# Optimization experiments

Measured on AMD Instinct MI355X. Metric: run time of the kernel, lower is better.

## Reference

```python
import jax, jax.numpy as jnp
import numpy as np

E = 512
H = 8
D = E // H
WIN = 128  # mask_window_size


def setup_inputs() -> dict:
    key = jax.random.key(0)
    k1, k2, k3, k4, k5 = jax.random.split(key, 5)
    B, L = 2, 4096
    s = 1.0 / np.sqrt(E)
    return {
        "x": jax.random.normal(k1, (B, L, E), dtype=jnp.float32),
        "in_proj_w": jax.random.normal(k2, (3 * E, E), dtype=jnp.float32) * s,
        "in_proj_b": jax.random.normal(k3, (3 * E,), dtype=jnp.float32) * 0.02,
        "out_w": jax.random.normal(k4, (E, E), dtype=jnp.float32) * s,
        "out_b": jax.random.normal(k5, (E,), dtype=jnp.float32) * 0.02,
    }


def reference(x, in_proj_w, in_proj_b, out_w, out_b):
    B, L, _ = x.shape
    # fused qkv projection (torch MultiheadAttention in_proj): x @ W.T + b
    qkv = jnp.einsum("ble,fe->blf", x, in_proj_w) + in_proj_b  # [B,L,3E]
    q, k, v = jnp.split(qkv, 3, axis=-1)
    # [B,H,L,D]
    q = q.reshape(B, L, H, D).transpose(0, 2, 1, 3)
    k = k.reshape(B, L, H, D).transpose(0, 2, 1, 3)
    v = v.reshape(B, L, H, D).transpose(0, 2, 1, 3)
    scores = jnp.einsum("bhqd,bhkd->bhqk", q, k) / jnp.sqrt(jnp.float32(D))
    # (diagonal stays blocked — faithful to the original gen_mask quirk)
    idx = jnp.arange(L)
    dist = jnp.abs(idx[:, None] - idx[None, :])
    blocked = (dist > WIN) | (dist == 0)  # [L,L]
    scores = jnp.where(blocked[None, None], -jnp.inf, scores)
    attn = jax.nn.softmax(scores, axis=-1)  # [B,H,L,L]
    out = jnp.einsum("bhqk,bhkd->bhqd", attn, v)  # [B,H,L,D]
    out = out.transpose(0, 2, 1, 3).reshape(B, L, E)
    return jnp.einsum("ble,fe->blf", out, out_w) + out_b
```

## Files before the change

### kernel.cpp

```cpp
#include <hip/hip_runtime.h>
#include <math.h>

#define E_DIM 512
#define H_DIM 8
#define WIN 128
#define L_SEQ 4096
#define B_SZ 2

typedef unsigned short ushort_t;
typedef unsigned int uint_t;
typedef __attribute__((ext_vector_type(8))) __bf16 bf16x8;
typedef __attribute__((ext_vector_type(4))) float f32x4;

__device__ __forceinline__ ushort_t f2bf(float f) {
    uint_t u = __float_as_uint(f);
    u = u + 0x7fffu + ((u >> 16) & 1u);
    return (ushort_t)(u >> 16);
}
__device__ __forceinline__ uint_t pk2bf(float lo, float hi) {
    uint_t r;
    asm("v_cvt_pk_bf16_f32 %0, %1, %2" : "=v"(r) : "v"(lo), "v"(hi));
    return r;
}

__device__ __forceinline__ void gload16(const ushort_t* g, ushort_t* l) {
    __builtin_amdgcn_global_load_lds(
        (const __attribute__((address_space(1))) void*)g,
        (__attribute__((address_space(3))) void*)l,
        16, 0, 0);
}


__global__ __launch_bounds__(256) void convertX(
    const float* __restrict__ x,  ushort_t* __restrict__ xh,
    const float* __restrict__ w1, ushort_t* __restrict__ w1h,
    const float* __restrict__ w2, ushort_t* __restrict__ w2h) {
    int sg = blockIdx.x * 256 + threadIdx.x;
    const float* src; ushort_t* dh;
    if (sg < 524288)      { src = x;  dh = xh; }
    else if (sg < 622592) { src = w1; dh = w1h; sg -= 524288; }
    else                  { src = w2; dh = w2h; sg -= 622592; }
    const int tile = sg >> 6, slot = sg & 63;
    const int row = (tile >> 4) * 16 + (slot & 15);
    const int k   = (tile & 15) * 32 + (slot >> 4) * 8;
    const float4 v0 = *(const float4*)&src[(size_t)row * 512 + k];
    const float4 v1 = *(const float4*)&src[(size_t)row * 512 + k + 4];
    uint4 ov;
    ov.x = pk2bf(v0.x, v0.y);
    ov.y = pk2bf(v0.z, v0.w);
    ov.z = pk2bf(v1.x, v1.y);
    ov.w = pk2bf(v1.z, v1.w);
    *(uint4*)(dh + (size_t)sg * 8) = ov;
}

__global__ __launch_bounds__(256) void gemm_qkv(
    const ushort_t* __restrict__ Ah,
    const ushort_t* __restrict__ Wh,
    const float* __restrict__ bias,
    ushort_t* __restrict__ qTh,
    ushort_t* __restrict__ kTh,
    ushort_t* __restrict__ vTh) {
    __shared__ __align__(16) ushort_t sAh[2][8 * 512];
    __shared__ __align__(16) ushort_t sWh[2][8 * 512];

    const int tid = threadIdx.x, lane = tid & 63, w = tid >> 6;
    const int wm = w & 1, wn = w >> 1, ln = lane & 15, quad = lane >> 4;
    const int bx = blockIdx.x, by = blockIdx.y;
    const int lo8 = lane * 8;
    const int wu = __builtin_amdgcn_readfirstlane(w);

    f32x4 acc[4][4];
    const f32x4 zero = {0.f, 0.f, 0.f, 0.f};
    #pragma unroll
    for (int i = 0; i < 4; i++)
        #pragma unroll
        for (int j = 0; j < 4; j++) acc[i][j] = zero;

    const ushort_t* pb[4];
    ushort_t* db0[4];
    ushort_t* db1[4];
    #pragma unroll
    for (int t = 0; t < 4; t++) {
        const int g = wu * 4 + t;
        if (g < 8) {
            pb[t] = Ah + ((size_t)(bx * 8 + g) * 16) * 512;
            db0[t] = &sAh[0][g * 512]; db1[t] = &sAh[1][g * 512];
        } else {
            const int u = g - 8;
            pb[t] = Wh + ((size_t)(by * 8 + u) * 16) * 512;
            db0[t] = &sWh[0][u * 512]; db1[t] = &sWh[1][u * 512];
        }
    }

    #pragma unroll
    for (int t = 0; t < 4; t++)
        gload16(pb[t] + lo8, db0[t]);

    for (int kt = 0; kt < 16; kt++) {
        __syncthreads();
        if (kt < 15) {
            const int koff = (kt + 1) * 512;
            if ((kt + 1) & 1) {
                #pragma unroll
                for (int t = 0; t < 4; t++) gload16(pb[t] + koff + lo8, db1[t]);
            } else {
                #pragma unroll
                for (int t = 0; t < 4; t++) gload16(pb[t] + koff + lo8, db0[t]);
            }
        }
        const int cb = kt & 1;
        bf16x8 fah[4];
        #pragma unroll
        for (int i = 0; i < 4; i++)
            fah[i] = *(const bf16x8*)&sAh[cb][(wm * 4 + i) * 512 + lo8];
        #pragma unroll
        for (int j = 0; j < 4; j++) {
            const bf16x8 fbh = *(const bf16x8*)&sWh[cb][(wn * 4 + j) * 512 + lo8];
            #pragma unroll
            for (int i = 0; i < 4; i++)
                acc[i][j] = __builtin_amdgcn_mfma_f32_16x16x32_bf16(fah[i], fbh, acc[i][j], 0, 0, 0);
        }
    }

    const int b = bx >> 5;
    const int h = 2 * (by & 3) + wn;
    if (by < 8) {
        ushort_t* dh = (by < 4) ? qTh : kTh;
        #pragma unroll
        for (int i = 0; i < 4; i++) {
            const int rt = (bx & 31) * 8 + wm * 4 + i;
            const size_t tb = ((size_t)(b * 8 + h) * 256 + rt) * 2;
            #pragma unroll
            for (int j = 0; j < 4; j++) {
                const float bv = bias[by * 128 + wn * 64 + j * 16 + ln];
                const size_t tile = tb + (j >> 1);
                const uint_t pa = pk2bf(acc[i][j][0] + bv, acc[i][j][1] + bv);
                const uint_t pc = pk2bf(acc[i][j][2] + bv, acc[i][j][3] + bv);
                const int slot0 = ((j * 2 + (ln >> 3)) & 3) * 16 + quad * 4;
                const size_t idx0 = tile * 512 + slot0 * 8 + (ln & 7);
                dh[idx0]      = (ushort_t)pa;
                dh[idx0 + 8]  = (ushort_t)(pa >> 16);
                dh[idx0 + 16] = (ushort_t)pc;
                dh[idx0 + 24] = (ushort_t)(pc >> 16);
            }
        }
    } else {
        const int kwin = (bx & 31) * 2 + wm;
        #pragma unroll
        for (int i = 0; i < 4; i++) {
            const int kk = i >> 1;
            #pragma unroll
            for (int j = 0; j < 4; j++) {
                const float bv = bias[by * 128 + wn * 64 + j * 16 + ln];
                const size_t tile = (((size_t)(b * 8 + h) * 64 + kwin) * 4 + j) * 2 + kk;
                const uint_t pa = pk2bf(acc[i][j][0] + bv, acc[i][j][1] + bv);
                const uint_t pc = pk2bf(acc[i][j][2] + bv, acc[i][j][3] + bv);
                const int slot = ((i & 1) * 2 + (quad >> 1)) * 16 + ln;
                uint2 ov; ov.x = pa; ov.y = pc;
                *(uint2*)&vTh[tile * 512 + slot * 8 + (quad & 1) * 4] = ov;
            }
        }
    }
}

__global__ __launch_bounds__(512) void attn_mfma(
    const ushort_t* __restrict__ qTh,
    const ushort_t* __restrict__ kTh,
    const ushort_t* __restrict__ vTh,
    ushort_t* __restrict__ outh) {
    __shared__ __align__(16) ushort_t sKh[2][8 * 512];
    __shared__ __align__(16) ushort_t sV [2][8 * 512];
    __shared__ __align__(16) ushort_t sP [16 * 512];

    const int qs = blockIdx.x * 128;
    const int h = blockIdx.y, b = blockIdx.z;
    const int bh = b * 8 + h;
    const int tid = threadIdx.x, lane = tid & 63;
    const int w = tid >> 6, ln = lane & 15, quad = lane >> 4;
    const int lo8 = lane * 8;

    bf16x8 qf[2];
    {
        const size_t qt = ((size_t)bh * 256 + (qs >> 4) + w) * 2;
        qf[0] = *(const bf16x8*)(qTh + (qt + 0) * 512 + lo8);
        qf[1] = *(const bf16x8*)(qTh + (qt + 1) * 512 + lo8);
    }

    f32x4 oacc[4];
    const f32x4 zero = {0.f, 0.f, 0.f, 0.f};
    #pragma unroll
    for (int dt = 0; dt < 4; dt++) oacc[dt] = zero;
    float m_run = -1e30f, l_run = 0.f;

    const float cscale = 0.125f * 1.44269504f;
    const int qlo = qs + 16 * w;
    const int q = qlo + ln;
    const int lo_b = (q - WIN) < 0 ? 0 : (q - WIN);
    const int hi_b = (q + WIN) > (L_SEQ - 1) ? (L_SEQ - 1) : (q + WIN);

    {
        if (w < 4) {
            int st = (qs >> 4) - 8 + w;
            st = st < 0 ? 0 : (st > 255 ? 255 : st);
            const size_t kb = ((size_t)bh * 256 + st) * 2 * 512 + lo8;
            gload16(kTh + kb,       &sKh[0][(w * 2 + 0) * 512]);
            gload16(kTh + kb + 512, &sKh[0][(w * 2 + 1) * 512]);
        } else {
            const int u = w - 4;
            int vw = (qs >> 6) - 2;
            vw = vw < 0 ? 0 : (vw > 63 ? 63 : vw);
            const size_t vb = (((size_t)bh * 64 + vw) * 4 + u) * 2 * 512 + lo8;
            gload16(vTh + vb,       &sV[0][(u * 2 + 0) * 512]);
            gload16(vTh + vb + 512, &sV[0][(u * 2 + 1) * 512]);
        }
    }

    for (int kt = 0; kt < 6; kt++) {
        const int ks = qs - 128 + kt * 64;

        __syncthreads();

        if (kt < 5) {
            const int nb = (kt + 1) & 1;
            if (w < 4) {
                int st = (qs >> 4) - 8 + (kt + 1) * 4 + w;
                st = st < 0 ? 0 : (st > 255 ? 255 : st);
                const size_t kb = ((size_t)bh * 256 + st) * 2 * 512 + lo8;
                gload16(kTh + kb,       &sKh[nb][(w * 2 + 0) * 512]);
                gload16(kTh + kb + 512, &sKh[nb][(w * 2 + 1) * 512]);
            } else {
                const int u = w - 4;
                int vw = (qs >> 6) - 2 + kt + 1;
                vw = vw < 0 ? 0 : (vw > 63 ? 63 : vw);
                const size_t vb = (((size_t)bh * 64 + vw) * 4 + u) * 2 * 512 + lo8;
                gload16(vTh + vb,       &sV[nb][(u * 2 + 0) * 512]);
                gload16(vTh + vb + 512, &sV[nb][(u * 2 + 1) * 512]);
            }
        }
        const int cb = kt & 1;

        bool dead[4];
        #pragma unroll
        for (int jt = 0; jt < 4; jt++) {
            const int klo = ks + 16 * jt;
            dead[jt] = (klo > qlo + 15 + WIN) || (klo + 15 < qlo - WIN) ||
                       (klo >= L_SEQ) || (klo + 15 < 0);
        }
        const bool hdead0 = dead[0] && dead[1];
        const bool hdead1 = dead[2] && dead[3];
        const bool ktAlive = !(hdead0 && hdead1);

        if (ktAlive) {
            f32x4 st4[4];
            __builtin_amdgcn_s_setprio(1);
            #pragma unroll
            for (int jt = 0; jt < 4; jt++) {
                f32x4 a = zero;
                if (!dead[jt]) {
                    #pragma unroll
                    for (int kk = 0; kk < 2; kk++) {
                        const bf16x8 kh = *(const bf16x8*)&sKh[cb][(jt * 2 + kk) * 512 + lo8];
                        a = __builtin_amdgcn_mfma_f32_16x16x32_bf16(kh, qf[kk], a, 0, 0, 0);
                    }
                }
                st4[jt] = a;
            }
            __builtin_amdgcn_s_setprio(0);

            float mkr = -INFINITY;
            #pragma unroll
            for (int jt = 0; jt < 4; jt++)
                if (!dead[jt])
                    #pragma unroll
                    for (int r = 0; r < 4; r++)
                        mkr = fmaxf(mkr, st4[jt][r]);
            mkr = fmaxf(mkr, __shfl_xor(mkr, 16));
            mkr = fmaxf(mkr, __shfl_xor(mkr, 32));

            const float mnew = fmaxf(m_run, mkr * cscale);
            const bool raised = mnew > m_run;
            const float alpha = exp2f(m_run - mnew);
            m_run = mnew;

            float ps = 0.f;
            #pragma unroll
            for (int jt = 0; jt < 4; jt++) {
                if (!dead[jt]) {
                    #pragma unroll
                    for (int r = 0; r < 4; r++) {
                        const int kcol = ks + jt * 16 + quad * 4 + r;
                        const bool ok = (kcol >= lo_b) && (kcol <= hi_b) && (kcol != q);
                        float p = exp2f(st4[jt][r] * cscale - mnew);
                        p = ok ? p : 0.f;
                        st4[jt][r] = p;
                        ps += p;
                    }
                }
            }
            ps += __shfl_xor(ps, 16);
            ps += __shfl_xor(ps, 32);
            l_run = l_run * alpha + ps;

            if (__any(raised)) {
                float ar[4];
                #pragma unroll
                for (int r = 0; r < 4; r++)
                    ar[r] = __shfl(alpha, quad * 4 + r);
                #pragma unroll
                for (int dt = 0; dt < 4; dt++)
                    #pragma unroll
                    for (int r = 0; r < 4; r++)
                        oacc[dt][r] *= ar[r];
            }

            #pragma unroll
            for (int jt = 0; jt < 4; jt++) {
                const bool hd = (jt < 2) ? hdead0 : hdead1;
                if (!hd) {
                    uint2 pw;
                    if (!dead[jt]) {
                        pw.x = pk2bf(st4[jt][0], st4[jt][1]);
                        pw.y = pk2bf(st4[jt][2], st4[jt][3]);
                    } else { pw.x = 0u; pw.y = 0u; }
                    const int slot = ((jt & 1) * 2 + (quad >> 1)) * 16 + ln;
                    *(uint2*)&sP[w * 1024 + (jt >> 1) * 512 + slot * 8 + (quad & 1) * 4] = pw;
                }
            }

            #pragma unroll
            for (int kk = 0; kk < 2; kk++) {
                const bool hd = (kk == 0) ? hdead0 : hdead1;
                if (!hd) {
                    const bf16x8 pf = *(const bf16x8*)&sP[w * 1024 + kk * 512 + lo8];
                    __builtin_amdgcn_s_setprio(1);
                    #pragma unroll
                    for (int dt = 0; dt < 4; dt++) {
                        const bf16x8 vf = *(const bf16x8*)&sV[cb][(dt * 2 + kk) * 512 + lo8];
                        oacc[dt] = __builtin_amdgcn_mfma_f32_16x16x32_bf16(pf, vf, oacc[dt], 0, 0, 0);
                    }
                    __builtin_amdgcn_s_setprio(0);
                }
            }
        }
    }

    const int Rt = ((b * L_SEQ + qs) >> 4) + w;
    float invl[4];
    #pragma unroll
    for (int r = 0; r < 4; r++) {
        const float lr = __shfl(l_run, quad * 4 + r);
        invl[r] = __builtin_amdgcn_rcpf(lr);
    }
    #pragma unroll
    for (int dt = 0; dt < 4; dt++) {
        const uint_t pa = pk2bf(oacc[dt][0] * invl[0], oacc[dt][1] * invl[1]);
        const uint_t pc = pk2bf(oacc[dt][2] * invl[2], oacc[dt][3] * invl[3]);
        const int tile = Rt * 16 + h * 2 + (dt >> 1);
        const int slot0 = ((dt & 1) * 2 + (ln >> 3)) * 16 + quad * 4;
        const size_t idx0 = (size_t)tile * 512 + slot0 * 8 + (ln & 7);
        outh[idx0]      = (ushort_t)pa;
        outh[idx0 + 8]  = (ushort_t)(pa >> 16);
        outh[idx0 + 16] = (ushort_t)pc;
        outh[idx0 + 24] = (ushort_t)(pc >> 16);
    }
}

__global__ __launch_bounds__(512) void gemm_out(
    const ushort_t* __restrict__ Ah,
    const ushort_t* __restrict__ Wh,
    const float* __restrict__ bias, float* __restrict__ C) {
    __shared__ __align__(16) ushort_t sAh[2][16 * 512];
    __shared__ __align__(16) ushort_t sWh[2][8 * 512];

    const int tid = threadIdx.x, lane = tid & 63, w = tid >> 6;
    const int wm = w & 3, wn = w >> 2, ln = lane & 15, quad = lane >> 4;
    const int bx = blockIdx.x, by = blockIdx.y;
    const int lo8 = lane * 8;
    const int wu = __builtin_amdgcn_readfirstlane(w);

    f32x4 acc[2][2];
    const f32x4 zero = {0.f, 0.f, 0.f, 0.f};
    #pragma unroll
    for (int i = 0; i < 2; i++)
        #pragma unroll
        for (int j = 0; j < 2; j++) acc[i][j] = zero;

    const ushort_t* pb[3];
    ushort_t* db0[3];
    ushort_t* db1[3];
    #pragma unroll
    for (int t = 0; t < 3; t++) {
        const int g = wu * 3 + t;
        if (g < 16) {
            pb[t] = Ah + ((size_t)(bx * 8 + (g >> 1)) * 16 + (g & 1)) * 512;
            db0[t] = &sAh[0][g * 512]; db1[t] = &sAh[1][g * 512];
        } else {
            const int u = g - 16;
            pb[t] = Wh + ((size_t)(by * 4 + (u >> 1)) * 16 + (u & 1)) * 512;
            db0[t] = &sWh[0][u * 512]; db1[t] = &sWh[1][u * 512];
        }
    }

    #pragma unroll
    for (int t = 0; t < 3; t++)
        gload16(pb[t] + lo8, db0[t]);

    for (int KT = 0; KT < 8; KT++) {
        __syncthreads();
        if (KT < 7) {
            const int koff = (KT + 1) * 1024;
            if ((KT + 1) & 1) {
                #pragma unroll
                for (int t = 0; t < 3; t++) gload16(pb[t] + koff + lo8, db1[t]);
            } else {
                #pragma unroll
                for (int t = 0; t < 3; t++) gload16(pb[t] + koff + lo8, db0[t]);
            }
        }
        const int cb = KT & 1;
        #pragma unroll
        for (int ks = 0; ks < 2; ks++) {
            bf16x8 fah[2];
            #pragma unroll
            for (int i = 0; i < 2; i++)
                fah[i] = *(const bf16x8*)&sAh[cb][((wm * 2 + i) * 2 + ks) * 512 + lo8];
            #pragma unroll
            for (int j = 0; j < 2; j++) {
                const bf16x8 fbh = *(const bf16x8*)&sWh[cb][((wn * 2 + j) * 2 + ks) * 512 + lo8];
                #pragma unroll
                for (int i = 0; i < 2; i++)
                    acc[i][j] = __builtin_amdgcn_mfma_f32_16x16x32_bf16(fah[i], fbh, acc[i][j], 0, 0, 0);
            }
        }
    }

    #pragma unroll
    for (int i = 0; i < 2; i++) {
        const int row0 = bx * 128 + wm * 32 + i * 16 + quad * 4;
        #pragma unroll
        for (int j = 0; j < 2; j++) {
            const int col = by * 64 + wn * 32 + j * 16 + ln;
            const float bv = bias[col];
            #pragma unroll
            for (int r = 0; r < 4; r++)
                C[(size_t)(row0 + r) * E_DIM + col] = acc[i][j][r] + bv;
        }
    }
}

extern "C" void kernel_launch(void* const* d_in, const int* in_sizes, int n_in,
                              void* d_out, int out_size, void* d_ws, size_t ws_size,
                              hipStream_t stream) {
    const float* x         = (const float*)d_in[0];
    const float* in_proj_w = (const float*)d_in[1];
    const float* in_proj_b = (const float*)d_in[2];
    const float* out_w     = (const float*)d_in[3];
    const float* out_b     = (const float*)d_in[4];
    float* out = (float*)d_out;

    const int N = B_SZ * L_SEQ;
    const size_t NE = (size_t)N * E_DIM;

    char* p = (char*)d_ws;
    ushort_t* xh  = (ushort_t*)p; p += NE * 2;
    ushort_t* w1h = (ushort_t*)p; p += (size_t)3 * E_DIM * E_DIM * 2;
    ushort_t* w2h = (ushort_t*)p; p += (size_t)E_DIM * E_DIM * 2;
    ushort_t* qTh = (ushort_t*)p; p += NE * 2;
    ushort_t* kTh = (ushort_t*)p; p += NE * 2;
    ushort_t* vTh = (ushort_t*)p; p += NE * 2;
    ushort_t* ath = (ushort_t*)p; p += NE * 2;

    convertX<<<2560, 256, 0, stream>>>(x, xh, in_proj_w, w1h, out_w, w2h);

    gemm_qkv<<<dim3(64, 12), 256, 0, stream>>>(
        xh, w1h, in_proj_b, qTh, kTh, vTh);

    attn_mfma<<<dim3(L_SEQ / 128, H_DIM, B_SZ), 512, 0, stream>>>(
        qTh, kTh, vTh, ath);

    gemm_out<<<dim3(64, 8), 512, 0, stream>>>(
        ath, w2h, out_b, out);
}
```

Baseline: 130.6 us.

## Triple-buffer LDS loads in QKV and output GEMMs with explicit vmcnt waits

Both projection GEMMs move from double to triple buffering in shared memory, prefetching two K-tiles ahead. The blanket __syncthreads is replaced with a partial s_waitcnt vmcnt wait followed by s_barrier, so the load of the tile after next stays in flight while the current tile is computed. This is meant to hide more global-to-LDS latency. It costs 50% more LDS per block, which may lower occupancy, and the hand-tuned vmcnt counts must exactly match how many loads each thread issues.

Measured after the change: 127.1 us. 2.7% less time.

```diff
diff --git a/kernel.cpp b/kernel.cpp
--- a/kernel.cpp
+++ b/kernel.cpp
@@ -60,8 +60,8 @@
     ushort_t* __restrict__ qTh,
     ushort_t* __restrict__ kTh,
     ushort_t* __restrict__ vTh) {
-    __shared__ __align__(16) ushort_t sAh[2][8 * 512];
-    __shared__ __align__(16) ushort_t sWh[2][8 * 512];
+    __shared__ __align__(16) ushort_t sAh[3][8 * 512];
+    __shared__ __align__(16) ushort_t sWh[3][8 * 512];
 
     const int tid = threadIdx.x, lane = tid & 63, w = tid >> 6;
     const int wm = w & 1, wn = w >> 1, ln = lane & 15, quad = lane >> 4;
@@ -69,6 +69,10 @@
     const int lo8 = lane * 8;
     const int wu = __builtin_amdgcn_readfirstlane(w);
 
+    const ushort_t* sA0 = &sAh[0][0];
+    const ushort_t* sW0 = &sWh[0][0];
+    const int BUF = 8 * 512;
+
     f32x4 acc[4][4];
     const f32x4 zero = {0.f, 0.f, 0.f, 0.f};
     #pragma unroll
@@ -77,45 +81,51 @@
         for (int j = 0; j < 4; j++) acc[i][j] = zero;
 
     const ushort_t* pb[4];
-    ushort_t* db0[4];
-    ushort_t* db1[4];
+    ushort_t* db[4];
     #pragma unroll
     for (int t = 0; t < 4; t++) {
         const int g = wu * 4 + t;
         if (g < 8) {
             pb[t] = Ah + ((size_t)(bx * 8 + g) * 16) * 512;
-            db0[t] = &sAh[0][g * 512]; db1[t] = &sAh[1][g * 512];
+            db[t] = &sAh[0][g * 512];
         } else {
             const int u = g - 8;
             pb[t] = Wh + ((size_t)(by * 8 + u) * 16) * 512;
-            db0[t] = &sWh[0][u * 512]; db1[t] = &sWh[1][u * 512];
-        }
-    }
-
-    #pragma unroll
-    for (int t = 0; t < 4; t++)
-        gload16(pb[t] + lo8, db0[t]);
-
+            db[t] = &sWh[0][u * 512];
+        }
+    }
+
+    #pragma unroll
+    for (int t = 0; t < 4; t++) gload16(pb[t] + lo8, db[t]);
+    #pragma unroll
+    for (int t = 0; t < 4; t++) gload16(pb[t] + 512 + lo8, db[t] + BUF);
+
+    int bw = 2, br = 0;
     for (int kt = 0; kt < 16; kt++) {
-        __syncthreads();
-        if (kt < 15) {
-            const int koff = (kt + 1) * 512;
-            if ((kt + 1) & 1) {
-                #pragma unroll
-                for (int t = 0; t < 4; t++) gload16(pb[t] + koff + lo8, db1[t]);
-            } else {
-                #pragma unroll
-                for (int t = 0; t < 4; t++) gload16(pb[t] + koff + lo8, db0[t]);
-            }
-        }
-        const int cb = kt & 1;
+        if (kt < 15) asm volatile("s_waitcnt vmcnt(4) lgkmcnt(0)" ::: "memory");
+        else         asm volatile("s_waitcnt vmcnt(0) lgkmcnt(0)" ::: "memory");
+        __builtin_amdgcn_s_barrier();
+        __builtin_amdgcn_sched_barrier(0);
+
+        if (kt < 14) {
+            const int koff = (kt + 2) * 512;
+            const int bwo = bw * BUF;
+            #pragma unroll
+            for (int t = 0; t < 4; t++)
+                gload16(pb[t] + koff + lo8, db[t] + bwo);
+            bw = (bw == 2) ? 0 : bw + 1;
+        }
+
+        const int bro = br * BUF;
+        br = (br == 2) ? 0 : br + 1;
+
         bf16x8 fah[4];
         #pragma unroll
         for (int i = 0; i < 4; i++)
-            fah[i] = *(const bf16x8*)&sAh[cb][(wm * 4 + i) * 512 + lo8];
+            fah[i] = *(const bf16x8*)&sA0[bro + (wm * 4 + i) * 512 + lo8];
         #pragma unroll
         for (int j = 0; j < 4; j++) {
-            const bf16x8 fbh = *(const bf16x8*)&sWh[cb][(wn * 4 + j) * 512 + lo8];
+            const bf16x8 fbh = *(const bf16x8*)&sW0[bro + (wn * 4 + j) * 512 + lo8];
             #pragma unroll
             for (int i = 0; i < 4; i++)
                 acc[i][j] = __builtin_amdgcn_mfma_f32_16x16x32_bf16(fah[i], fbh, acc[i][j], 0, 0, 0);
@@ -369,8 +379,8 @@
     const ushort_t* __restrict__ Ah,
     const ushort_t* __restrict__ Wh,
     const float* __restrict__ bias, float* __restrict__ C) {
-    __shared__ __align__(16) ushort_t sAh[2][16 * 512];
-    __shared__ __align__(16) ushort_t sWh[2][8 * 512];
+    __shared__ __align__(16) ushort_t sAh[3][16 * 512];
+    __shared__ __align__(16) ushort_t sWh[3][8 * 512];
 
     const int tid = threadIdx.x, lane = tid & 63, w = tid >> 6;
     const int wm = w & 3, wn = w >> 2, ln = lane & 15, quad = lane >> 4;
@@ -378,6 +388,10 @@
     const int lo8 = lane * 8;
     const int wu = __builtin_amdgcn_readfirstlane(w);
 
+    const ushort_t* sA0 = &sAh[0][0];
+    const ushort_t* sW0 = &sWh[0][0];
+    const int BUFA = 16 * 512, BUFW = 8 * 512;
+
     f32x4 acc[2][2];
     const f32x4 zero = {0.f, 0.f, 0.f, 0.f};
     #pragma unroll
@@ -386,47 +400,53 @@
         for (int j = 0; j < 2; j++) acc[i][j] = zero;
 
     const ushort_t* pb[3];
-    ushort_t* db0[3];
-    ushort_t* db1[3];
+    ushort_t* db[3];
+    int ds[3];
     #pragma unroll
     for (int t = 0; t < 3; t++) {
         const int g = wu * 3 + t;
         if (g < 16) {
             pb[t] = Ah + ((size_t)(bx * 8 + (g >> 1)) * 16 + (g & 1)) * 512;
-            db0[t] = &sAh[0][g * 512]; db1[t] = &sAh[1][g * 512];
+            db[t] = &sAh[0][g * 512]; ds[t] = BUFA;
         } else {
             const int u = g - 16;
             pb[t] = Wh + ((size_t)(by * 4 + (u >> 1)) * 16 + (u & 1)) * 512;
-            db0[t] = &sWh[0][u * 512]; db1[t] = &sWh[1][u * 512];
-        }
-    }
-
-    #pragma unroll
-    for (int t = 0; t < 3; t++)
-        gload16(pb[t] + lo8, db0[t]);
-
+            db[t] = &sWh[0][u * 512]; ds[t] = BUFW;
+        }
+    }
+
+    #pragma unroll
+    for (int t = 0; t < 3; t++) gload16(pb[t] + lo8, db[t]);
+    #pragma unroll
+    for (int t = 0; t < 3; t++) gload16(pb[t] + 1024 + lo8, db[t] + ds[t]);
+
+    int bw = 2, br = 0;
     for (int KT = 0; KT < 8; KT++) {
-        __syncthreads();
-        if (KT < 7) {
-            const int koff = (KT + 1) * 1024;
-            if ((KT + 1) & 1) {
-                #pragma unroll
-                for (int t = 0; t < 3; t++) gload16(pb[t] + koff + lo8, db1[t]);
-            } else {
-                #pragma unroll
-                for (int t = 0; t < 3; t++) gload16(pb[t] + koff + lo8, db0[t]);
-            }
-        }
-        const int cb = KT & 1;
+        if (KT < 7) asm volatile("s_waitcnt vmcnt(3) lgkmcnt(0)" ::: "memory");
+        else        asm volatile("s_waitcnt vmcnt(0) lgkmcnt(0)" ::: "memory");
+        __builtin_amdgcn_s_barrier();
+        __builtin_amdgcn_sched_barrier(0);
+
+        if (KT < 6) {
+            const int koff = (KT + 2) * 1024;
+            #pragma unroll
+            for (int t = 0; t < 3; t++)
+                gload16(pb[t] + koff + lo8, db[t] + bw * ds[t]);
+            bw = (bw == 2) ? 0 : bw + 1;
+        }
+
+        const int broA = br * BUFA, broW = br * BUFW;
+        br = (br == 2) ? 0 : br + 1;
+
         #pragma unroll
         for (int ks = 0; ks < 2; ks++) {
             bf16x8 fah[2];
             #pragma unroll
             for (int i = 0; i < 2; i++)
-                fah[i] = *(const bf16x8*)&sAh[cb][((wm * 2 + i) * 2 + ks) * 512 + lo8];
+                fah[i] = *(const bf16x8*)&sA0[broA + ((wm * 2 + i) * 2 + ks) * 512 + lo8];
             #pragma unroll
             for (int j = 0; j < 2; j++) {
-                const bf16x8 fbh = *(const bf16x8*)&sWh[cb][((wn * 2 + j) * 2 + ks) * 512 + lo8];
+                const bf16x8 fbh = *(const bf16x8*)&sW0[broW + ((wn * 2 + j) * 2 + ks) * 512 + lo8];
                 #pragma unroll
                 for (int i = 0; i < 2; i++)
                     acc[i][j] = __builtin_amdgcn_mfma_f32_16x16x32_bf16(fah[i], fbh, acc[i][j], 0, 0, 0);
```
